# Kernel tuning notes

Hardware: AMD Instinct MI355X
Metric: run time of the kernel (lower is better)

The kernel has to match this reference:

```python
import jax, jax.numpy as jnp
import numpy as np

N_QUBITS = 9
N_LAYERS = 2
N_ACTIONS = 1
K = 3  # kernel size
DIM = 1 << N_QUBITS  # 512 state-vector length


def _apply_1q(state, mat, q):
    """Apply a 2x2 gate on wire q (wire 0 = most significant bit, PennyLane convention).
    state: (N, DIM) complex64. mat: (2,2) shared or (N,2,2) per-sample."""
    a = 1 << q
    b = 1 << (N_QUBITS - 1 - q)
    s = state.reshape(-1, a, 2, b)
    if mat.ndim == 2:
        out = jnp.einsum('ij,najb->naib', mat, s)
    else:
        out = jnp.einsum('nij,najb->naib', mat, s)
    return out.reshape(state.shape)


def _cnot_perm(c, t):
    """Index permutation implementing CNOT(control=c, target=t) on the 512-dim basis."""
    idx = np.arange(DIM)
    cbit = (idx >> (N_QUBITS - 1 - c)) & 1
    return np.where(cbit == 1, idx ^ (1 << (N_QUBITS - 1 - t)), idx)


def _circuit(inputs, weights):
    """Batched state-vector simulation of: AngleEmbedding(RX) + StronglyEntanglingLayers.
    inputs: (N, 9) float. weights: (n_layers, 9, 3) float. Returns (N, N_ACTIONS) expval PauliZ."""
    N = inputs.shape[0]
    state = jnp.zeros((N, DIM), jnp.complex64).at[:, 0].set(1.0)

    # AngleEmbedding: RX(x_q) on each wire (per-sample angles)
    half = inputs.astype(jnp.float32) * 0.5
    c = jnp.cos(half).astype(jnp.complex64)
    s = (-1j * jnp.sin(half)).astype(jnp.complex64)
    for q in range(N_QUBITS):
        row0 = jnp.stack([c[:, q], s[:, q]], axis=-1)
        row1 = jnp.stack([s[:, q], c[:, q]], axis=-1)
        mat = jnp.stack([row0, row1], axis=-2)  # (N,2,2)
        state = _apply_1q(state, mat, q)

    # StronglyEntanglingLayers: per layer, Rot on each wire then CNOT ring of range r
    for l in range(N_LAYERS):
        phi, theta, omega = weights[l, :, 0], weights[l, :, 1], weights[l, :, 2]
        ct = jnp.cos(theta * 0.5).astype(jnp.complex64)
        st = jnp.sin(theta * 0.5).astype(jnp.complex64)
        ep = jnp.exp(-0.5j * (phi + omega).astype(jnp.complex64))  # e^{-i(phi+omega)/2}
        em = jnp.exp(0.5j * (phi - omega).astype(jnp.complex64))   # e^{+i(phi-omega)/2}
        for q in range(N_QUBITS):
            # Rot(phi,theta,omega) = RZ(omega) RY(theta) RZ(phi)
            mat = jnp.stack([
                jnp.stack([ep[q] * ct[q], -em[q] * st[q]]),
                jnp.stack([jnp.conj(em[q]) * st[q], jnp.conj(ep[q]) * ct[q]]),
            ]).astype(jnp.complex64)
            state = _apply_1q(state, mat, q)
        r = (l % (N_QUBITS - 1)) + 1  # PennyLane default ranges
        for q in range(N_QUBITS):
            state = state[:, _cnot_perm(q, (q + r) % N_QUBITS)]

    probs = state.real ** 2 + state.imag ** 2  # (N, DIM)
    idx = np.arange(DIM)
    exps = []
    for w in range(N_ACTIONS):
        z = (1.0 - 2.0 * ((idx >> (N_QUBITS - 1 - w)) & 1)).astype(np.float32)
        exps.append(probs @ jnp.asarray(z))
    return jnp.stack(exps, axis=-1)  # (N, N_ACTIONS)


def setup_inputs() -> dict:
    key = jax.random.key(0)
    k1, k2 = jax.random.split(key)
    x = jax.random.normal(k1, (8, 1, 64, 64), dtype=jnp.float32)
    # TorchLayer default init: uniform in [0, 2*pi)
    weights = jax.random.uniform(k2, (N_LAYERS, N_QUBITS, 3), dtype=jnp.float32) * (2.0 * np.pi)
    return {"x": x, "weights": weights}


def reference(x, weights):
    b, ch, h, w = x.shape
    # unfold(kernel=3, padding=1): patch feature k = ki*3+kj taken at (i+ki-1, j+kj-1)
    xp = jnp.pad(x, ((0, 0), (0, 0), (1, 1), (1, 1)))
    patches = jnp.stack(
        [xp[:, 0, ki:ki + h, kj:kj + w] for ki in range(K) for kj in range(K)],
        axis=-1,
    )  # (B, H, W, 9) -- matches unfold().transpose(1,2).reshape(-1,9) row order
    inputs = patches.reshape(-1, K * K)
    q_out = _circuit(inputs, weights)          # (B*H*W, n_actions)
    return q_out.reshape(b, h, w, -1).transpose(0, 3, 1, 2)  # (B, n_actions, H, W)
```

## Files before the change

kernel.cpp:

```cpp
#include <hip/hip_runtime.h>


#if defined(__clang__)
#pragma float_control(precise, off)
#endif

struct C2 { float r, i; };
__device__ __forceinline__ C2 cmul(C2 a, C2 b) {
    return C2{a.r * b.r - a.i * b.i, a.r * b.i + a.i * b.r};
}
__device__ __forceinline__ C2 cadd(C2 a, C2 b) { return C2{a.r + b.r, a.i + b.i}; }

template<int C8BASE, int NC8>
__device__ __forceinline__ float dp_eval(const float (&Zb)[9], const float (&Xb)[9],
                                         const float (&Yb)[9], const float (&hm)[5][3]) {
    C2 F[9][2][2];
    #pragma unroll
    for (int m = 0; m < 9; ++m) {
        F[m][0][0] = C2{1.0f, 0.0f};
        F[m][1][0] = C2{Zb[m], 0.0f};
        F[m][0][1] = C2{Xb[m], 0.0f};
        F[m][1][1] = C2{0.0f, Yb[m]};
    }
    C2 K[5][3];
    #pragma unroll
    for (int i = 0; i < 5; ++i) {
        K[i][0] = C2{hm[i][0], 0.0f};
        K[i][1] = C2{hm[i][1], 0.0f};
        K[i][2] = C2{0.0f, hm[i][2]};
    }
    const int A[3] = {1, 0, 1};
    const int B[3] = {0, 1, 1};

    C2 S7[2][NC8];
    #pragma unroll
    for (int t5 = 0; t5 < 2; ++t5) {
        #pragma unroll
        for (int c8i = 0; c8i < NC8; ++c8i) {
            const int c8 = C8BASE + c8i;
            const int a8 = A[c8], b8 = B[c8];
            C2 acc = C2{0.0f, 0.0f};
            #pragma unroll
            for (int c7 = 0; c7 < 3; ++c7) {
                const int a7 = A[c7], b7 = B[c7];
                C2 v = cmul(K[1][c7], F[6][t5][b7]);
                v = cmul(v, F[7][t5 ^ a7][b7 ^ b8]);
                v = cmul(v, F[8][t5 ^ a8 ^ a7][b8]);
                acc = cadd(acc, v);
            }
            S7[t5][c8i] = acc;
        }
    }
    C2 S5[2][NC8];
    #pragma unroll
    for (int t3 = 0; t3 < 2; ++t3) {
        #pragma unroll
        for (int c8i = 0; c8i < NC8; ++c8i) {
            C2 acc = C2{0.0f, 0.0f};
            #pragma unroll
            for (int c5 = 0; c5 < 3; ++c5) {
                const int a5 = A[c5], b5 = B[c5];
                C2 v = cmul(K[2][c5], F[4][t3][b5]);
                v = cmul(v, F[5][t3 ^ a5][b5]);
                v = cmul(v, S7[t3 ^ a5][c8i]);
                acc = cadd(acc, v);
            }
            S5[t3][c8i] = acc;
        }
    }
    C2 S3[2][NC8];
    #pragma unroll
    for (int t1 = 0; t1 < 2; ++t1) {
        #pragma unroll
        for (int c8i = 0; c8i < NC8; ++c8i) {
            C2 acc = C2{0.0f, 0.0f};
            #pragma unroll
            for (int c3 = 0; c3 < 3; ++c3) {
                const int a3 = A[c3], b3 = B[c3];
                C2 v = cmul(K[3][c3], F[2][t1][b3]);
                v = cmul(v, F[3][t1 ^ a3][b3]);
                v = cmul(v, S5[t1 ^ a3][c8i]);
                acc = cadd(acc, v);
            }
            S3[t1][c8i] = acc;
        }
    }
    float E = 0.0f;
    #pragma unroll
    for (int c8i = 0; c8i < NC8; ++c8i) {
        const int c8 = C8BASE + c8i;
        const int a8 = A[c8];
        C2 acc = C2{0.0f, 0.0f};
        #pragma unroll
        for (int c1 = 0; c1 < 3; ++c1) {
            const int a1 = A[c1], b1 = B[c1];
            C2 v = cmul(K[4][c1], F[0][a8][b1]);
            v = cmul(v, F[1][a8 ^ a1][b1]);
            v = cmul(v, S3[a8 ^ a1][c8i]);
            acc = cadd(acc, v);
        }
        E += K[0][c8].r * acc.r - K[0][c8].i * acc.i;
    }
    return E;
}

__global__ __launch_bounds__(192) void qsim_kernel(const float* __restrict__ x,
                                                   const float* __restrict__ w,
                                                   float* __restrict__ out,
                                                   int nsamples) {
    __shared__ float cb[9][6];
    __shared__ float hm[5][3];
    __shared__ float part[2][64];
    const int tid = threadIdx.x;
    if (tid < 9) {
        const int q = tid;
        const float phi = w[q * 3 + 0], theta = w[q * 3 + 1], omega = w[q * 3 + 2];
        float st, ct, sp, cp, sm, cm;
        __sincosf(0.5f * theta, &st, &ct);
        __sincosf(0.5f * (phi + omega), &sp, &cp);
        __sincosf(0.5f * (phi - omega), &sm, &cm);
        const float m00r =  cp * ct, m00i = -sp * ct;
        const float m01r = -cm * st, m01i = -sm * st;
        const float m10r =  cm * st, m10i = -sm * st;
        const float m11r =  cp * ct, m11i =  sp * ct;
        cb[q][0] = (m00r * m00r + m00i * m00i) - (m10r * m10r + m10i * m10i);
        cb[q][2] = 2.0f * (m00r * m10r + m00i * m10i);
        cb[q][4] = 2.0f * (m00r * m10i - m00i * m10r);
        const float u0r = m00r - m01i, u0i = m00i + m01r;
        const float u1r = m10r - m11i, u1i = m10i + m11r;
        cb[q][1] = 0.5f * ((u0r * u0r + u0i * u0i) - (u1r * u1r + u1i * u1i));
        cb[q][3] = (u0r * u1r + u0i * u1i);
        cb[q][5] = (u0r * u1i - u0i * u1r);
    } else if (tid >= 16 && tid < 21) {
        const int i = tid - 16;
        const int qs[5] = {0, 1, 3, 5, 7};
        const int q = qs[i];
        const float phi = w[27 + q * 3 + 0], theta = w[27 + q * 3 + 1];
        float stt, ctt, sf, cf;
        __sincosf(theta, &stt, &ctt);
        __sincosf(phi, &sf, &cf);
        hm[i][0] = ctt;
        hm[i][1] = -stt * cf;
        hm[i][2] = -stt * sf;
    }
    __syncthreads();

    const int lane = tid & 63;
    const int wv = tid >> 6;
    const int n = (blockIdx.x << 6) + lane;

    float E = 0.0f;
    if (n < nsamples) {
        const int b  = n >> 12;
        const int i0 = (n >> 6) & 63;
        const int j0 = n & 63;

        float Zb[9], Xb[9], Yb[9];
        #pragma unroll
        for (int ki = 0; ki < 3; ++ki) {
            #pragma unroll
            for (int kj = 0; kj < 3; ++kj) {
                const int q = ki * 3 + kj;
                const int m = 8 - q;
                const int ii = i0 + ki - 1, jj = j0 + kj - 1;
                const bool ok = ((unsigned)ii < 64u) & ((unsigned)jj < 64u);
                float a = x[(b << 12) + ((ii & 63) << 6) + (jj & 63)];
                a = ok ? a : 0.0f;
                float sa, ca;
                __sincosf(a, &sa, &ca);
                Zb[m] = ca * cb[q][0] - sa * cb[q][1];
                Xb[m] = ca * cb[q][2] - sa * cb[q][3];
                Yb[m] = ca * cb[q][4] - sa * cb[q][5];
            }
        }
        if      (wv == 0) E = dp_eval<0, 1>(Zb, Xb, Yb, hm);
        else if (wv == 1) E = dp_eval<1, 1>(Zb, Xb, Yb, hm);
        else              E = dp_eval<2, 1>(Zb, Xb, Yb, hm);
    }
    if (wv) part[wv - 1][lane] = E;
    __syncthreads();
    if (wv == 0 && n < nsamples) out[n] = E + part[0][lane] + part[1][lane];
}

extern "C" void kernel_launch(void* const* d_in, const int* in_sizes, int n_in,
                              void* d_out, int out_size, void* d_ws, size_t ws_size,
                              hipStream_t stream) {
    const float* x = (const float*)d_in[0];
    const float* w = (const float*)d_in[1];
    float* out = (float*)d_out;
    const int nsamples = out_size;
    const int blocks = (nsamples + 63) >> 6;
    qsim_kernel<<<blocks, 192, 0, stream>>>(x, w, out, nsamples);
}
```

Before: 11.42 us.

## Factor tensor contraction into shared 2x2 transfer matrices, one thread per sample

Replaces the three-wave split of the c8 branches with a single thread per sample. The c8-independent middle and outer stages are factored into 2x2 transfer matrices (M5, M3, R) and contracted once into V, then combined with S7 for all three branches. This removes the redundant per-wave recomputation of the sin/cos patch setup and the shared-memory partial-sum reduction with its extra barrier. The cost is more live registers per thread and blocks of 256 samples instead of 64.

Measured after the change: 12.22 us. 1.07x slower.

```diff
diff --git a/kernel.cpp b/kernel.cpp
--- a/kernel.cpp
+++ b/kernel.cpp
@@ -11,106 +11,12 @@
 }
 __device__ __forceinline__ C2 cadd(C2 a, C2 b) { return C2{a.r + b.r, a.i + b.i}; }
 
-template<int C8BASE, int NC8>
-__device__ __forceinline__ float dp_eval(const float (&Zb)[9], const float (&Xb)[9],
-                                         const float (&Yb)[9], const float (&hm)[5][3]) {
-    C2 F[9][2][2];
-    #pragma unroll
-    for (int m = 0; m < 9; ++m) {
-        F[m][0][0] = C2{1.0f, 0.0f};
-        F[m][1][0] = C2{Zb[m], 0.0f};
-        F[m][0][1] = C2{Xb[m], 0.0f};
-        F[m][1][1] = C2{0.0f, Yb[m]};
-    }
-    C2 K[5][3];
-    #pragma unroll
-    for (int i = 0; i < 5; ++i) {
-        K[i][0] = C2{hm[i][0], 0.0f};
-        K[i][1] = C2{hm[i][1], 0.0f};
-        K[i][2] = C2{0.0f, hm[i][2]};
-    }
-    const int A[3] = {1, 0, 1};
-    const int B[3] = {0, 1, 1};
-
-    C2 S7[2][NC8];
-    #pragma unroll
-    for (int t5 = 0; t5 < 2; ++t5) {
-        #pragma unroll
-        for (int c8i = 0; c8i < NC8; ++c8i) {
-            const int c8 = C8BASE + c8i;
-            const int a8 = A[c8], b8 = B[c8];
-            C2 acc = C2{0.0f, 0.0f};
-            #pragma unroll
-            for (int c7 = 0; c7 < 3; ++c7) {
-                const int a7 = A[c7], b7 = B[c7];
-                C2 v = cmul(K[1][c7], F[6][t5][b7]);
-                v = cmul(v, F[7][t5 ^ a7][b7 ^ b8]);
-                v = cmul(v, F[8][t5 ^ a8 ^ a7][b8]);
-                acc = cadd(acc, v);
-            }
-            S7[t5][c8i] = acc;
-        }
-    }
-    C2 S5[2][NC8];
-    #pragma unroll
-    for (int t3 = 0; t3 < 2; ++t3) {
-        #pragma unroll
-        for (int c8i = 0; c8i < NC8; ++c8i) {
-            C2 acc = C2{0.0f, 0.0f};
-            #pragma unroll
-            for (int c5 = 0; c5 < 3; ++c5) {
-                const int a5 = A[c5], b5 = B[c5];
-                C2 v = cmul(K[2][c5], F[4][t3][b5]);
-                v = cmul(v, F[5][t3 ^ a5][b5]);
-                v = cmul(v, S7[t3 ^ a5][c8i]);
-                acc = cadd(acc, v);
-            }
-            S5[t3][c8i] = acc;
-        }
-    }
-    C2 S3[2][NC8];
-    #pragma unroll
-    for (int t1 = 0; t1 < 2; ++t1) {
-        #pragma unroll
-        for (int c8i = 0; c8i < NC8; ++c8i) {
-            C2 acc = C2{0.0f, 0.0f};
-            #pragma unroll
-            for (int c3 = 0; c3 < 3; ++c3) {
-                const int a3 = A[c3], b3 = B[c3];
-                C2 v = cmul(K[3][c3], F[2][t1][b3]);
-                v = cmul(v, F[3][t1 ^ a3][b3]);
-                v = cmul(v, S5[t1 ^ a3][c8i]);
-                acc = cadd(acc, v);
-            }
-            S3[t1][c8i] = acc;
-        }
-    }
-    float E = 0.0f;
-    #pragma unroll
-    for (int c8i = 0; c8i < NC8; ++c8i) {
-        const int c8 = C8BASE + c8i;
-        const int a8 = A[c8];
-        C2 acc = C2{0.0f, 0.0f};
-        #pragma unroll
-        for (int c1 = 0; c1 < 3; ++c1) {
-            const int a1 = A[c1], b1 = B[c1];
-            C2 v = cmul(K[4][c1], F[0][a8][b1]);
-            v = cmul(v, F[1][a8 ^ a1][b1]);
-            v = cmul(v, S3[a8 ^ a1][c8i]);
-            acc = cadd(acc, v);
-        }
-        E += K[0][c8].r * acc.r - K[0][c8].i * acc.i;
-    }
-    return E;
-}
-
-__global__ __launch_bounds__(192) void qsim_kernel(const float* __restrict__ x,
+__global__ __launch_bounds__(256) void qsim_kernel(const float* __restrict__ x,
                                                    const float* __restrict__ w,
                                                    float* __restrict__ out,
                                                    int nsamples) {
     __shared__ float cb[9][6];
     __shared__ float hm[5][3];
-    __shared__ float part[2][64];
     const int tid = threadIdx.x;
     if (tid < 9) {
         const int q = tid;
@@ -145,41 +51,104 @@
     }
     __syncthreads();
 
-    const int lane = tid & 63;
-    const int wv = tid >> 6;
-    const int n = (blockIdx.x << 6) + lane;
+    const int n = (blockIdx.x << 8) + tid;
+    if (n >= nsamples) return;
+    const int b  = n >> 12;
+    const int i0 = (n >> 6) & 63;
+    const int j0 = n & 63;
 
+    float Zb[9], Xb[9], Yb[9];
+    #pragma unroll
+    for (int ki = 0; ki < 3; ++ki) {
+        #pragma unroll
+        for (int kj = 0; kj < 3; ++kj) {
+            const int q = ki * 3 + kj;
+            const int m = 8 - q;
+            const int ii = i0 + ki - 1, jj = j0 + kj - 1;
+            const bool ok = ((unsigned)ii < 64u) & ((unsigned)jj < 64u);
+            float a = x[(b << 12) + ((ii & 63) << 6) + (jj & 63)];
+            a = ok ? a : 0.0f;
+            float sa, ca;
+            __sincosf(a, &sa, &ca);
+            Zb[m] = ca * cb[q][0] - sa * cb[q][1];
+            Xb[m] = ca * cb[q][2] - sa * cb[q][3];
+            Yb[m] = ca * cb[q][4] - sa * cb[q][5];
+        }
+    }
+
+    C2 F[9][2][2];
+    #pragma unroll
+    for (int m = 0; m < 9; ++m) {
+        F[m][0][0] = C2{1.0f, 0.0f};
+        F[m][1][0] = C2{Zb[m], 0.0f};
+        F[m][0][1] = C2{Xb[m], 0.0f};
+        F[m][1][1] = C2{0.0f, Yb[m]};
+    }
+    C2 K[5][3];
+    #pragma unroll
+    for (int i = 0; i < 5; ++i) {
+        K[i][0] = C2{hm[i][0], 0.0f};
+        K[i][1] = C2{hm[i][1], 0.0f};
+        K[i][2] = C2{0.0f, hm[i][2]};
+    }
+    const int A[3] = {1, 0, 1};
+    const int B[3] = {0, 1, 1};
+
+    C2 S7[2][3];
+    #pragma unroll
+    for (int t5 = 0; t5 < 2; ++t5) {
+        #pragma unroll
+        for (int c8 = 0; c8 < 3; ++c8) {
+            const int a8 = A[c8], b8 = B[c8];
+            C2 acc = C2{0.0f, 0.0f};
+            #pragma unroll
+            for (int c7 = 0; c7 < 3; ++c7) {
+                const int a7 = A[c7], b7 = B[c7];
+                C2 v = cmul(K[1][c7], F[6][t5][b7]);
+                v = cmul(v, F[7][t5 ^ a7][b7 ^ b8]);
+                v = cmul(v, F[8][t5 ^ a8 ^ a7][b8]);
+                acc = cadd(acc, v);
+            }
+            S7[t5][c8] = acc;
+        }
+    }
+
+    C2 M5[2][2], M3[2][2];
+    #pragma unroll
+    for (int t = 0; t < 2; ++t) {
+        M5[t][t]     = cmul(K[2][1], cmul(F[4][t][1], F[5][t][1]));
+        M5[t][t ^ 1] = cadd(cmul(K[2][0], cmul(F[4][t][0], F[5][t ^ 1][0])),
+                            cmul(K[2][2], cmul(F[4][t][1], F[5][t ^ 1][1])));
+        M3[t][t]     = cmul(K[3][1], cmul(F[2][t][1], F[3][t][1]));
+        M3[t][t ^ 1] = cadd(cmul(K[3][0], cmul(F[2][t][0], F[3][t ^ 1][0])),
+                            cmul(K[3][2], cmul(F[2][t][1], F[3][t ^ 1][1])));
+    }
+    C2 R[2][2];
+    #pragma unroll
+    for (int a8 = 0; a8 < 2; ++a8) {
+        R[a8][a8]     = cmul(K[4][1], cmul(F[0][a8][1], F[1][a8][1]));
+        R[a8][a8 ^ 1] = cadd(cmul(K[4][0], cmul(F[0][a8][0], F[1][a8 ^ 1][0])),
+                             cmul(K[4][2], cmul(F[0][a8][1], F[1][a8 ^ 1][1])));
+    }
+    C2 V[2][2];
+    #pragma unroll
+    for (int a8 = 0; a8 < 2; ++a8) {
+        C2 rm[2];
+        #pragma unroll
+        for (int t3 = 0; t3 < 2; ++t3)
+            rm[t3] = cadd(cmul(R[a8][0], M3[0][t3]), cmul(R[a8][1], M3[1][t3]));
+        #pragma unroll
+        for (int t5 = 0; t5 < 2; ++t5)
+            V[a8][t5] = cadd(cmul(rm[0], M5[0][t5]), cmul(rm[1], M5[1][t5]));
+    }
     float E = 0.0f;
-    if (n < nsamples) {
-        const int b  = n >> 12;
-        const int i0 = (n >> 6) & 63;
-        const int j0 = n & 63;
-
-        float Zb[9], Xb[9], Yb[9];
-        #pragma unroll
-        for (int ki = 0; ki < 3; ++ki) {
-            #pragma unroll
-            for (int kj = 0; kj < 3; ++kj) {
-                const int q = ki * 3 + kj;
-                const int m = 8 - q;
-                const int ii = i0 + ki - 1, jj = j0 + kj - 1;
-                const bool ok = ((unsigned)ii < 64u) & ((unsigned)jj < 64u);
-                float a = x[(b << 12) + ((ii & 63) << 6) + (jj & 63)];
-                a = ok ? a : 0.0f;
-                float sa, ca;
-                __sincosf(a, &sa, &ca);
-                Zb[m] = ca * cb[q][0] - sa * cb[q][1];
-                Xb[m] = ca * cb[q][2] - sa * cb[q][3];
-                Yb[m] = ca * cb[q][4] - sa * cb[q][5];
-            }
-        }
-        if      (wv == 0) E = dp_eval<0, 1>(Zb, Xb, Yb, hm);
-        else if (wv == 1) E = dp_eval<1, 1>(Zb, Xb, Yb, hm);
-        else              E = dp_eval<2, 1>(Zb, Xb, Yb, hm);
+    #pragma unroll
+    for (int c8 = 0; c8 < 3; ++c8) {
+        const int a8 = A[c8];
+        C2 acc = cadd(cmul(V[a8][0], S7[0][c8]), cmul(V[a8][1], S7[1][c8]));
+        E += K[0][c8].r * acc.r - K[0][c8].i * acc.i;
     }
-    if (wv) part[wv - 1][lane] = E;
-    __syncthreads();
-    if (wv == 0 && n < nsamples) out[n] = E + part[0][lane] + part[1][lane];
+    out[n] = E;
 }
 
 extern "C" void kernel_launch(void* const* d_in, const int* in_sizes, int n_in,
@@ -189,6 +158,6 @@
     const float* w = (const float*)d_in[1];
     float* out = (float*)d_out;
     const int nsamples = out_size;
-    const int blocks = (nsamples + 63) >> 6;
-    qsim_kernel<<<blocks, 192, 0, stream>>>(x, w, out, nsamples);
+    const int blocks = (nsamples + 255) >> 8;
+    qsim_kernel<<<blocks, 256, 0, stream>>>(x, w, out, nsamples);
 }
```
